# Performance work log

Measured on AMD Instinct MI355X. Metric: run time of the kernel, lower is better.

The kernel has to match this reference:

```python
import jax, jax.numpy as jnp
import numpy as np

THRESH = 0.5
RADIUS = 4  # maxpool kernel = 2*RADIUS+1 = 9


def setup_inputs() -> dict:
    key = jax.random.key(0)
    H = W = 8192
    pred_vol = jax.random.uniform(key, (H, W), dtype=jnp.float32)
    return {"pred_vol": pred_vol}


def reference(pred_vol):
    # Faithful translation of Postprocess.forward up through conf_vol
    # (the threshold + 9x9 local-max pooling + equality-compare peak map).
    # The original's torch.nonzero / numpy coordinate extraction is a
    # data-dependent-shape host-side epilogue and is not part of the
    # dense kernel; the dense conf_vol fully determines it.
    k = 2 * RADIUS + 1
    # threshold: keep values strictly above thresh, else 0
    pred_thresh = jnp.where(pred_vol > THRESH, pred_vol, 0.0)
    # local max pool, stride 1, SAME-style padding with -inf (matches
    # torch MaxPool2d implicit -inf padding)
    mp = jax.lax.reduce_window(
        pred_thresh,
        -jnp.inf,
        jax.lax.max,
        window_dimensions=(k, k),
        window_strides=(1, 1),
        padding=((RADIUS, RADIUS), (RADIUS, RADIUS)),
    )
    # keep only positions that are both positive and the local maximum
    conf_vol = jnp.where((mp > 0.0) & (mp == pred_thresh), mp, 0.0)
    return conf_vol
```

## Files before the change

kernel.cpp:

```cpp
#include <hip/hip_runtime.h>


#define H 8192
#define W 8192
#define TILE 64
#define HALO 4
#define INW (TILE + 2 * HALO)
#define THRESH 0.5f

__global__ __launch_bounds__(256) void peak9x9_kernel(const float* __restrict__ in,
                                                      float* __restrict__ out) {
    __shared__ float s_in[INW * INW];
    __shared__ float s_cm[TILE * INW];

    const int tid  = threadIdx.x;
    const int col0 = blockIdx.x * TILE;
    const int row0 = blockIdx.y * TILE;

    for (int i = tid; i < 72 * 18; i += 256) {
        const int rr = i / 18;
        const int f4 = i - rr * 18;
        const int gr = row0 - HALO + rr;
        const int gc = col0 - HALO + f4 * 4;
        float4 v;
        if ((unsigned)gr < (unsigned)H && (unsigned)gc < (unsigned)W) {
            v = *(const float4*)(in + (size_t)gr * W + gc);
        } else {
            v = make_float4(0.f, 0.f, 0.f, 0.f);
        }
        v.x = v.x > THRESH ? v.x : 0.f;
        v.y = v.y > THRESH ? v.y : 0.f;
        v.z = v.z > THRESH ? v.z : 0.f;
        v.w = v.w > THRESH ? v.w : 0.f;
        *(float4*)(&s_in[rr * INW + f4 * 4]) = v;
    }
    __syncthreads();

    {
        const int tx = tid & 63;
        const int ty = tid >> 6;
        const int r0 = ty * 16;
        for (int cc = tx; cc < INW; cc += 64) {
            float v[24];
#pragma unroll
            for (int i = 0; i < 24; ++i) v[i] = s_in[(r0 + i) * INW + cc];
#pragma unroll
            for (int r = 0; r < 16; ++r) {
                float m = v[r];
#pragma unroll
                for (int j = 1; j < 9; ++j) m = fmaxf(m, v[r + j]);
                s_cm[(r0 + r) * INW + cc] = m;
            }
        }
    }
    __syncthreads();

    {
        const int cg = tid & 15;
        const int rb = tid >> 4;
        const int c0 = cg * 4;
#pragma unroll
        for (int k = 0; k < 4; ++k) {
            const int r = rb + k * 16;
            const float4 va = *(const float4*)&s_cm[r * INW + c0];
            const float4 vb = *(const float4*)&s_cm[r * INW + c0 + 4];
            const float4 vc = *(const float4*)&s_cm[r * INW + c0 + 8];
            const float common = fmaxf(fmaxf(fmaxf(va.w, vb.x), fmaxf(vb.y, vb.z)),
                                       fmaxf(vb.w, vc.x));
            const float m12  = fmaxf(va.y, va.z);
            const float m910 = fmaxf(vc.y, vc.z);
            const float o0 = fmaxf(common, fmaxf(va.x, m12));
            const float o1 = fmaxf(common, fmaxf(m12, vc.y));
            const float o2 = fmaxf(common, fmaxf(va.z, m910));
            const float o3 = fmaxf(common, fmaxf(m910, vc.w));
            const float4 pt = *(const float4*)&s_in[(r + 4) * INW + c0 + 4];
            float4 ov;
            ov.x = (o0 > 0.f && o0 == pt.x) ? o0 : 0.f;
            ov.y = (o1 > 0.f && o1 == pt.y) ? o1 : 0.f;
            ov.z = (o2 > 0.f && o2 == pt.z) ? o2 : 0.f;
            ov.w = (o3 > 0.f && o3 == pt.w) ? o3 : 0.f;
            *(float4*)(out + (size_t)(row0 + r) * W + (col0 + c0)) = ov;
        }
    }
}

extern "C" void kernel_launch(void* const* d_in, const int* in_sizes, int n_in,
                              void* d_out, int out_size, void* d_ws, size_t ws_size,
                              hipStream_t stream) {
    const float* in = (const float*)d_in[0];
    float* out = (float*)d_out;
    dim3 grid(W / TILE, H / TILE);
    peak9x9_kernel<<<grid, dim3(256, 1, 1), 0, stream>>>(in, out);
}
```

Measured before the change: 441.9 us.

## Replace shared-memory tiled 9x9 peak detection with register-streaming row sweep

```diff
diff --git a/kernel.cpp b/kernel.cpp
--- a/kernel.cpp
+++ b/kernel.cpp
@@ -1,85 +1,75 @@
 #include <hip/hip_runtime.h>
 
 
+#define W 8192
 #define H 8192
-#define W 8192
-#define TILE 64
-#define HALO 4
-#define INW (TILE + 2 * HALO)
 #define THRESH 0.5f
 
-__global__ __launch_bounds__(256) void peak9x9_kernel(const float* __restrict__ in,
+typedef float v4f __attribute__((ext_vector_type(4)));
+
+__device__ __forceinline__ v4f ld4(const float* __restrict__ in, int r, int c) {
+    v4f v = {0.f, 0.f, 0.f, 0.f};
+    if ((unsigned)c < (unsigned)W) {
+        v = *(const v4f*)(in + (size_t)r * W + c);
+    }
+    return v;
+}
+
+__global__ __launch_bounds__(256, 4) void peak_stream(const float* __restrict__ in,
                                                       float* __restrict__ out) {
-    __shared__ float s_in[INW * INW];
-    __shared__ float s_cm[TILE * INW];
+    const int lane = threadIdx.x;
+    const int col0 = blockIdx.x * 256 + lane * 4;
+    const int r0   = (blockIdx.y * 4 + threadIdx.y) * 64;
 
-    const int tid  = threadIdx.x;
-    const int col0 = blockIdx.x * TILE;
-    const int row0 = blockIdx.y * TILE;
+    v4f hm[9];
+    v4f ce[9];
 
-    for (int i = tid; i < 72 * 18; i += 256) {
-        const int rr = i / 18;
-        const int f4 = i - rr * 18;
-        const int gr = row0 - HALO + rr;
-        const int gc = col0 - HALO + f4 * 4;
-        float4 v;
-        if ((unsigned)gr < (unsigned)H && (unsigned)gc < (unsigned)W) {
-            v = *(const float4*)(in + (size_t)gr * W + gc);
-        } else {
-            v = make_float4(0.f, 0.f, 0.f, 0.f);
+    auto dorow = [&](int rin, int k, bool emit) {
+        v4f l = {0.f, 0.f, 0.f, 0.f}, v = l, r = l;
+        if ((unsigned)rin < (unsigned)H) {
+            l = ld4(in, rin, col0 - 4);
+            v = ld4(in, rin, col0);
+            r = ld4(in, rin, col0 + 4);
         }
-        v.x = v.x > THRESH ? v.x : 0.f;
-        v.y = v.y > THRESH ? v.y : 0.f;
-        v.z = v.z > THRESH ? v.z : 0.f;
-        v.w = v.w > THRESH ? v.w : 0.f;
-        *(float4*)(&s_in[rr * INW + f4 * 4]) = v;
+        const float common = fmaxf(fmaxf(fmaxf(l.w, v.x), fmaxf(v.y, v.z)),
+                                   fmaxf(v.w, r.x));
+        const float m12  = fmaxf(l.y, l.z);
+        const float m910 = fmaxf(r.y, r.z);
+        v4f o;
+        o.x = fmaxf(common, fmaxf(l.x, m12));
+        o.y = fmaxf(common, fmaxf(m12, r.y));
+        o.z = fmaxf(common, fmaxf(l.z, m910));
+        o.w = fmaxf(common, fmaxf(m910, r.w));
+        hm[k] = o;
+        ce[k] = v;
+        if (emit) {
+            v4f m = hm[0];
+#pragma unroll
+            for (int j = 1; j < 9; ++j) {
+                m.x = fmaxf(m.x, hm[j].x);
+                m.y = fmaxf(m.y, hm[j].y);
+                m.z = fmaxf(m.z, hm[j].z);
+                m.w = fmaxf(m.w, hm[j].w);
+            }
+            const v4f c4 = ce[(k + 5) % 9];
+            v4f ov;
+            ov.x = (m.x > THRESH && m.x == c4.x) ? m.x : 0.f;
+            ov.y = (m.y > THRESH && m.y == c4.y) ? m.y : 0.f;
+            ov.z = (m.z > THRESH && m.z == c4.z) ? m.z : 0.f;
+            ov.w = (m.w > THRESH && m.w == c4.w) ? m.w : 0.f;
+            const int rout = rin - 4;
+            *(v4f*)(out + (size_t)rout * W + col0) = ov;
+        }
+    };
+
+#pragma unroll
+    for (int t = 0; t < 9; ++t) {
+        dorow(r0 - 4 + t, t, t >= 8);
     }
-    __syncthreads();
-
-    {
-        const int tx = tid & 63;
-        const int ty = tid >> 6;
-        const int r0 = ty * 16;
-        for (int cc = tx; cc < INW; cc += 64) {
-            float v[24];
+    for (int tc = 9; tc < 72; tc += 9) {
 #pragma unroll
-            for (int i = 0; i < 24; ++i) v[i] = s_in[(r0 + i) * INW + cc];
-#pragma unroll
-            for (int r = 0; r < 16; ++r) {
-                float m = v[r];
-#pragma unroll
-                for (int j = 1; j < 9; ++j) m = fmaxf(m, v[r + j]);
-                s_cm[(r0 + r) * INW + cc] = m;
-            }
-        }
-    }
-    __syncthreads();
-
-    {
-        const int cg = tid & 15;
-        const int rb = tid >> 4;
-        const int c0 = cg * 4;
-#pragma unroll
-        for (int k = 0; k < 4; ++k) {
-            const int r = rb + k * 16;
-            const float4 va = *(const float4*)&s_cm[r * INW + c0];
-            const float4 vb = *(const float4*)&s_cm[r * INW + c0 + 4];
-            const float4 vc = *(const float4*)&s_cm[r * INW + c0 + 8];
-            const float common = fmaxf(fmaxf(fmaxf(va.w, vb.x), fmaxf(vb.y, vb.z)),
-                                       fmaxf(vb.w, vc.x));
-            const float m12  = fmaxf(va.y, va.z);
-            const float m910 = fmaxf(vc.y, vc.z);
-            const float o0 = fmaxf(common, fmaxf(va.x, m12));
-            const float o1 = fmaxf(common, fmaxf(m12, vc.y));
-            const float o2 = fmaxf(common, fmaxf(va.z, m910));
-            const float o3 = fmaxf(common, fmaxf(m910, vc.w));
-            const float4 pt = *(const float4*)&s_in[(r + 4) * INW + c0 + 4];
-            float4 ov;
-            ov.x = (o0 > 0.f && o0 == pt.x) ? o0 : 0.f;
-            ov.y = (o1 > 0.f && o1 == pt.y) ? o1 : 0.f;
-            ov.z = (o2 > 0.f && o2 == pt.z) ? o2 : 0.f;
-            ov.w = (o3 > 0.f && o3 == pt.w) ? o3 : 0.f;
-            *(float4*)(out + (size_t)(row0 + r) * W + (col0 + c0)) = ov;
+        for (int k = 0; k < 9; ++k) {
+            dorow(r0 - 4 + tc + k, k, true);
         }
     }
 }
@@ -89,6 +79,7 @@
                               hipStream_t stream) {
     const float* in = (const float*)d_in[0];
     float* out = (float*)d_out;
-    dim3 grid(W / TILE, H / TILE);
-    peak9x9_kernel<<<grid, dim3(256, 1, 1), 0, stream>>>(in, out);
+    dim3 grid(W / 256, H / 256);
+    dim3 block(64, 4, 1);
+    peak_stream<<<grid, block, 0, stream>>>(in, out);
 }
```

New measurement: 440.9 us. No clear change (-0.2%).
